# Kernel optimization log

Hardware: AMD Instinct MI355X
Metric: run time of the kernel (lower is better)

Reference implementation:

```python
import jax, jax.numpy as jnp
import numpy as np

B, C_ENC, H, W = 8, 512, 96, 96
N_SAMP = 64            # num_samples in forward
N_NODES = 2 * N_SAMP   # 64 pos + 64 neg per image
D = 256                # node feature dim after head_in_ln
N_HEADS = 8
DH = D // N_HEADS
SINKHORN_ITERS = 10


def _ln(x):
    # LayerNorm(elementwise_affine=False)
    m = x.mean(-1, keepdims=True)
    v = x.var(-1, keepdims=True)
    return (x - m) / jnp.sqrt(v + 1e-5)


def setup_inputs() -> dict:
    key = jax.random.key(0)
    ks = jax.random.split(key, 12)
    std = 0.01  # matches nn.init.normal_(std=0.01) in _init_weights
    inp = {
        "feat_s": jax.random.normal(ks[0], (B, C_ENC, H, W), jnp.float32),
        "score_s": jax.random.normal(ks[1], (B, 1, H, W), jnp.float32),
        "feat_t": jax.random.normal(ks[2], (B, C_ENC, H, W), jnp.float32),
        "score_t": jax.random.normal(ks[3], (B, 1, H, W), jnp.float32),
        "head_W1": std * jax.random.normal(ks[4], (C_ENC, D), jnp.float32),
        "head_b1": jnp.zeros((D,), jnp.float32),
        "head_W2": std * jax.random.normal(ks[5], (D, D), jnp.float32),
        "head_b2": jnp.zeros((D,), jnp.float32),
        "intra_W": jax.random.normal(ks[6], (4, D, D), jnp.float32) / jnp.sqrt(jnp.float32(D)),
        "intra_b": jnp.zeros((4, D), jnp.float32),
        "cross_W": jax.random.normal(ks[7], (4, D, D), jnp.float32) / jnp.sqrt(jnp.float32(D)),
        "cross_b": jnp.zeros((4, D), jnp.float32),
        "cls_W1": std * jax.random.normal(ks[8], (D, 128), jnp.float32),
        "cls_b1": jnp.zeros((128,), jnp.float32),
        "cls_W2": std * jax.random.normal(ks[9], (128, 1), jnp.float32),
        "cls_b2": jnp.zeros((1,), jnp.float32),
        "aff_A": jax.random.normal(ks[10], (D, D), jnp.float32) / jnp.sqrt(jnp.float32(D)),
    }
    return inp


def _sample_points(feat, score):
    # torch version: boolean-mask nonzero + random gather of 64 pos / 64 neg spatial
    # locations per image. JIT-friendly deterministic equivalent: top-64 highest
    # sigmoid scores = positives, top-64 lowest = negatives.
    s = jax.nn.sigmoid(score[:, 0].reshape(B, -1))            # [B, H*W]
    _, pos_idx = jax.lax.top_k(s, N_SAMP)
    _, neg_idx = jax.lax.top_k(-s, N_SAMP)
    idx = jnp.concatenate([pos_idx, neg_idx], axis=1)         # [B, 128]
    ff = feat.reshape(B, C_ENC, -1)                           # [B, 512, H*W]
    nodes = jnp.take_along_axis(ff, idx[:, None, :], axis=2)  # [B, 512, 128]
    nodes = nodes.transpose(0, 2, 1)                          # [B, 128, 512]
    labels = jnp.concatenate(
        [jnp.ones((B, N_SAMP, 1), feat.dtype), jnp.zeros((B, N_SAMP, 1), feat.dtype)], axis=1)
    return nodes, labels


def _mha(xq, xkv, Wp, bp):
    # standard multi-head attention (MultiHeadAttentionWrapper)
    q = xq @ Wp[0] + bp[0]
    k = xkv @ Wp[1] + bp[1]
    v = xkv @ Wp[2] + bp[2]
    sh = lambda t: t.reshape(t.shape[0], t.shape[1], N_HEADS, DH)
    att = jnp.einsum("bqhd,bkhd->bhqk", sh(q), sh(k)) / jnp.sqrt(jnp.float32(DH))
    att = jax.nn.softmax(att, axis=-1)
    o = jnp.einsum("bhqk,bkhd->bqhd", att, sh(v)).reshape(xq.shape[0], xq.shape[1], D)
    return o @ Wp[3] + bp[3], att.mean(1)


def _forward(feat_s, score_s, feat_t, score_t, head_W1, head_b1, head_W2, head_b2,
             intra_W, intra_b, cross_W, cross_b, cls_W1, cls_b1, cls_W2, cls_b2, aff_A):
    n1, l1 = _sample_points(feat_s, score_s)
    n2, l2 = _sample_points(feat_t, score_t)

    # head_in_ln: Linear -> LN -> ReLU -> Linear -> LN
    head = lambda x: _ln(jax.nn.relu(_ln(x @ head_W1 + head_b1)) @ head_W2 + head_b2)
    n1, n2 = head(n1), head(n2)

    # intra-domain graph (self-attention), shared weights for both domains
    n1, _ = _mha(n1, n1, intra_W, intra_b)
    n2, _ = _mha(n2, n2, intra_W, intra_b)

    # cross-domain graph (cross-attention both directions, shared weights)
    c1, _ = _mha(n1, n2, cross_W, cross_b)
    c2, _ = _mha(n2, n1, cross_W, cross_b)
    n1, n2 = c1, c2

    # node classification loss (BCEWithLogits, mean)
    cls = lambda x: jax.nn.relu(x @ cls_W1 + cls_b1) @ cls_W2 + cls_b2
    def bce_logits(logit, lab):
        return jnp.mean(jnp.maximum(logit, 0) - logit * lab + jnp.log1p(jnp.exp(-jnp.abs(logit))))
    node_loss = bce_logits(cls(n1), l1) + bce_logits(cls(n2), l2)

    # affinity + InstanceNorm2d(1) + sinkhorn refine
    Mmat = jnp.einsum("bnd,de,bme->bnm", n1, aff_A, n2)       # [B, 128, 128]
    mu = Mmat.mean((1, 2), keepdims=True)
    var = Mmat.var((1, 2), keepdims=True)
    K = (Mmat - mu) / jnp.sqrt(var + 1e-5)
    for _ in range(SINKHORN_ITERS):  # log-space row/col normalization
        K = K - jax.nn.logsumexp(K, axis=2, keepdims=True)
        K = K - jax.nn.logsumexp(K, axis=1, keepdims=True)
    P = jnp.exp(K)

    # matching loss = BCEFocalLoss(gamma=2, alpha=0.25) vs label-agreement matrix
    gt = (l1[:, :, 0][:, :, None] == l2[:, :, 0][:, None, :]).astype(P.dtype)
    pt = jnp.clip(P, 1e-6, 1.0 - 1e-6)
    mat_loss = jnp.mean(-0.25 * (1 - pt) ** 2 * gt * jnp.log(pt)
                        - 0.75 * pt ** 2 * (1 - gt) * jnp.log(1 - pt))

    total_loss = node_loss + 10.0 * mat_loss
    return n1, total_loss


def reference(feat_s, score_s, feat_t, score_t, head_W1, head_b1, head_W2, head_b2,
              intra_W, intra_b, cross_W, cross_b, cls_W1, cls_b1, cls_W2, cls_b2, aff_A):
    return _forward(feat_s, score_s, feat_t, score_t, head_W1, head_b1, head_W2, head_b2,
                    intra_W, intra_b, cross_W, cross_b, cls_W1, cls_b1, cls_W2, cls_b2, aff_A)
```

## Files before the change

kernel.cpp:

```cpp
#include <hip/hip_runtime.h>
#include <math.h>

#define BIMG 8
#define HW 9216
#define CENC 512
#define NN 128
#define DD 256
#define NHEAD 8
#define DH 32
#define ROWS1 1024
#define ROWS2 2048
#define TAILB 264

typedef unsigned long long ull;
typedef __attribute__((ext_vector_type(4))) float f32x4;
typedef __attribute__((ext_vector_type(4))) unsigned u32x4;
typedef __attribute__((ext_vector_type(2))) unsigned u32x2;

__device__ __forceinline__ unsigned short f2bf(float f) {
  unsigned u = __float_as_uint(f);
  u += 0x7fffu + ((u >> 16) & 1u);
  return (unsigned short)(u >> 16);
}
__device__ __forceinline__ float bf2f(unsigned h) { return __uint_as_float(h << 16); }
__device__ __forceinline__ unsigned pack2(float a, float b) {
  return (unsigned)f2bf(a) | ((unsigned)f2bf(b) << 16);
}

__device__ __forceinline__ ull cmpex_keep(ull k, ull o, bool keepMax) {
  return ((k > o) == keepMax) ? k : o;
}
__device__ __forceinline__ void bsort64(ull& k, int lane) {
#pragma unroll
  for (int size = 2; size <= 64; size <<= 1) {
#pragma unroll
    for (int stride = size >> 1; stride > 0; stride >>= 1) {
      ull o = __shfl_xor(k, stride);
      bool keepMax = (((lane & size) == 0) == ((lane & stride) == 0));
      k = cmpex_keep(k, o, keepMax);
    }
  }
}
__device__ __forceinline__ void bmerge64(ull& top, ull b, int lane) {
  ull rev = __shfl_xor(b, 63);
  ull m = top > rev ? top : rev;
#pragma unroll
  for (int stride = 32; stride > 0; stride >>= 1) {
    ull o = __shfl_xor(m, stride);
    m = cmpex_keep(m, o, (lane & stride) == 0);
  }
  top = m;
}

__global__ __launch_bounds__(256) void head_kernel(const float* __restrict__ score_s,
                                                   const float* __restrict__ score_t,
                                                   int* __restrict__ idx_out,
                                                   float* __restrict__ loss_acc,
                                                   const float* __restrict__ hw1,
                                                   const float* __restrict__ hw2,
                                                   const float* __restrict__ iw,
                                                   const float* __restrict__ cw,
                                                   const float* __restrict__ aw,
                                                   unsigned short* __restrict__ wt) {
  __shared__ ull sm[256];
  __shared__ float tile[32][33];
  int tid = threadIdx.x;
  if (blockIdx.x < 32) {
    int blk = blockIdx.x;
    int bi = blk >> 1, neg = blk & 1;
    int lane = tid & 63, w = tid >> 6;
    if (blk == 0 && tid < 4) loss_acc[tid] = 0.f;
    const float* sp = (bi < 8 ? score_s : score_t) + (size_t)(bi & 7) * HW;
    int q0 = w * 36;
    ull keys[36];
#pragma unroll
    for (int j = 0; j < 36; ++j) {
      float x = sp[(q0 + j) * 64 + lane];
      unsigned ub = __float_as_uint(x);
      unsigned u = (ub & 0x80000000u) ? ~ub : (ub | 0x80000000u);
      if (neg) u = ~u;
      int gi = (q0 + j) * 64 + lane;
      keys[j] = ((ull)u << 32) | (unsigned)(~gi);
    }
    ull top1 = keys[0];  bsort64(top1, lane);
    ull top2 = keys[18]; bsort64(top2, lane);
#pragma unroll
    for (int j = 1; j < 18; ++j) {
      ull k1 = keys[j], k2 = keys[18 + j];
      bsort64(k1, lane);
      bsort64(k2, lane);
      bmerge64(top1, k1, lane);
      bmerge64(top2, k2, lane);
    }
    bmerge64(top1, top2, lane);
    sm[w * 64 + lane] = top1;
    __syncthreads();
    if (w < 2) {
      ull a = sm[(2 * w) * 64 + lane];
      ull b = sm[(2 * w + 1) * 64 + (63 - lane)];
      ull m = a > b ? a : b;
#pragma unroll
      for (int stride = 32; stride > 0; stride >>= 1) {
        ull o = __shfl_xor(m, stride);
        m = cmpex_keep(m, o, (lane & stride) == 0);
      }
      sm[(2 * w) * 64 + lane] = m;
    }
    __syncthreads();
    if (w == 0) {
      ull a = sm[lane];
      ull b = sm[128 + (63 - lane)];
      ull m = a > b ? a : b;
#pragma unroll
      for (int stride = 32; stride > 0; stride >>= 1) {
        ull o = __shfl_xor(m, stride);
        m = cmpex_keep(m, o, (lane & stride) == 0);
      }
      idx_out[bi * NN + neg * 64 + lane] = (int)(~(unsigned)(m & 0xffffffffull));
    }
  } else {
    int bid = blockIdx.x - 32;
    const float* src; unsigned short* dst; int K, k0, n0;
    if (bid < 128) {
      src = hw1; dst = wt; K = 512;
      k0 = (bid >> 3) * 32; n0 = (bid & 7) * 32;
    } else {
      int id2 = bid - 128;
      int m = id2 >> 6, tt = id2 & 63;
      K = 256;
      k0 = (tt >> 3) * 32; n0 = (tt & 7) * 32;
      src = (m == 0) ? hw2 : (m < 5) ? iw + (size_t)(m - 1) * 65536
          : (m < 9) ? cw + (size_t)(m - 5) * 65536 : aw;
      dst = wt + 131072 + (size_t)m * 65536;
    }
    int r = tid >> 3, c = (tid & 7) * 4;
    float4 v = *(const float4*)&src[(size_t)(k0 + r) * 256 + n0 + c];
    tile[r][c] = v.x; tile[r][c + 1] = v.y; tile[r][c + 2] = v.z; tile[r][c + 3] = v.w;
    __syncthreads();
    u32x2 o;
    o[0] = pack2(tile[c][r], tile[c + 1][r]);
    o[1] = pack2(tile[c + 2][r], tile[c + 3][r]);
    *(u32x2*)&dst[(size_t)(n0 + r) * K + k0 + c] = o;
  }
}

__global__ __launch_bounds__(256) void gather_kernel(const float* __restrict__ feat_s,
                                                     const float* __restrict__ feat_t,
                                                     const int* __restrict__ idx,
                                                     unsigned short* __restrict__ nodes) {
  int blk = blockIdx.x;
  int bi = blk >> 7, n = blk & 127;
  int b = bi & 7;
  const float* fp = (bi < 8) ? feat_s : feat_t;
  int pos = idx[bi * NN + n];
  const float* src = fp + (size_t)b * CENC * HW + pos;
  unsigned* dst = (unsigned*)(nodes + (size_t)blk * CENC);
  int t = threadIdx.x;
  float f0 = src[(size_t)(2 * t) * HW];
  float f1 = src[(size_t)(2 * t + 1) * HW];
  dst[t] = pack2(f0, f1);
}

template<int K>
__global__ __launch_bounds__(256) void gemm_mf(const unsigned short* __restrict__ A,
                                               const unsigned short* __restrict__ Wt,
                                               const float* __restrict__ bias,
                                               unsigned short* __restrict__ Cb,
                                               float* __restrict__ Cf,
                                               int ldc, int f32rows,
                                               const float* __restrict__ in_stats, int in_relu,
                                               float* __restrict__ out_stats,
                                               int Az, int Wz, int Cbz, int Cfz, int bz) {
  constexpr int LDK = K + 8;
  constexpr int KC = K / 8;
  __shared__ unsigned short As[32][LDK];
  __shared__ unsigned short Bs[64][LDK];
  __shared__ float mS[32], rS[32];
  int z = blockIdx.z;
  A  += (size_t)z * Az;
  Wt += (size_t)z * Wz;
  if (Cb)   Cb += (size_t)z * Cbz;
  if (Cf)   Cf += (size_t)z * Cfz;
  if (bias) bias += (size_t)z * bz;
  int n0 = blockIdx.x * 64, m0 = blockIdx.y * 32;
  int t = threadIdx.x;
  if (in_stats) {
    if (t < 32) {
      const float* sp = in_stats + (size_t)(m0 + t) * 16;
      float s = 0.f, q = 0.f;
#pragma unroll
      for (int i = 0; i < 8; ++i) { s += sp[i]; q += sp[8 + i]; }
      float m = s * (1.0f / 256.f);
      float var = q * (1.0f / 256.f) - m * m;
      mS[t] = m;
      rS[t] = 1.0f / sqrtf(var + 1e-5f);
    }
    __syncthreads();
  }
  for (int i = t; i < 32 * KC; i += 256) {
    int row = i / KC, c8 = (i % KC) * 8;
    u32x4 av = *(const u32x4*)&A[(size_t)(m0 + row) * K + c8];
    if (in_stats) {
      float m = mS[row], r = rS[row];
#pragma unroll
      for (int j = 0; j < 4; ++j) {
        float f0 = (bf2f(av[j] & 0xffffu) - m) * r;
        float f1 = (bf2f(av[j] >> 16) - m) * r;
        if (in_relu) { f0 = fmaxf(f0, 0.f); f1 = fmaxf(f1, 0.f); }
        av[j] = pack2(f0, f1);
      }
    }
    *(u32x4*)&As[row][c8] = av;
  }
  for (int i = t; i < 64 * KC; i += 256) {
    int row = i / KC, c8 = (i % KC) * 8;
    *(u32x4*)&Bs[row][c8] = *(const u32x4*)&Wt[(size_t)(n0 + row) * K + c8];
  }
  __syncthreads();
  int l = t & 63, w = t >> 6;
  int wr = w >> 1, wc = w & 1;
  int fra = wr * 16 + (l & 15);
  int frk = (l >> 4) * 8;
  int fb0 = wc * 32 + (l & 15), fb1 = fb0 + 16;
  f32x4 acc0 = {0.f, 0.f, 0.f, 0.f};
  f32x4 acc1 = {0.f, 0.f, 0.f, 0.f};
#pragma unroll
  for (int ks = 0; ks < K / 32; ++ks) {
    u32x4 af = *(const u32x4*)&As[fra][ks * 32 + frk];
    u32x4 b0 = *(const u32x4*)&Bs[fb0][ks * 32 + frk];
    u32x4 b1 = *(const u32x4*)&Bs[fb1][ks * 32 + frk];
    asm volatile("v_mfma_f32_16x16x32_bf16 %0, %1, %2, %0" : "+v"(acc0) : "v"(af), "v"(b0));
    asm volatile("v_mfma_f32_16x16x32_bf16 %0, %1, %2, %0" : "+v"(acc1) : "v"(af), "v"(b1));
  }
  asm volatile("s_nop 7\n\ts_nop 7" ::);
  int col0 = n0 + wc * 32 + (l & 15);
  int rbase = m0 + wr * 16 + (l >> 4) * 4;
  float b0 = 0.f, b1 = 0.f;
  if (bias) { b0 = bias[col0]; b1 = bias[col0 + 16]; }
#pragma unroll
  for (int r = 0; r < 4; ++r) {
    int row = rbase + r;
    float o0 = acc0[r] + b0;
    float o1 = acc1[r] + b1;
    if (Cb) {
      Cb[(size_t)row * 256 + col0]      = f2bf(o0);
      Cb[(size_t)row * 256 + col0 + 16] = f2bf(o1);
    }
    if (Cf && row < f32rows) {
      Cf[(size_t)row * ldc + col0]      = o0;
      Cf[(size_t)row * ldc + col0 + 16] = o1;
    }
    if (out_stats) {
      float s = o0 + o1, q = o0 * o0 + o1 * o1;
#pragma unroll
      for (int m = 1; m < 16; m <<= 1) { s += __shfl_xor(s, m); q += __shfl_xor(q, m); }
      if ((l & 15) == 0) {
        out_stats[(size_t)row * 16 + blockIdx.x * 2 + wc]     = s;
        out_stats[(size_t)row * 16 + 8 + blockIdx.x * 2 + wc] = q;
      }
    }
  }
}

__global__ __launch_bounds__(256) void attn_kernel(const unsigned short* __restrict__ q,
                                                   const unsigned short* __restrict__ k,
                                                   const unsigned short* __restrict__ v,
                                                   unsigned short* __restrict__ o, int swap) {
  __shared__ __align__(16) float Ks[NN][DH];
  __shared__ __align__(16) float Vs[NN][DH];
  __shared__ __align__(16) float Ex[64][3][34];
  int blk = blockIdx.x;
  int bb = blk >> 4, h = (blk >> 1) & 7, qh = blk & 1;
  int kb = swap ? (bb ^ 8) : bb;
  int t = threadIdx.x;
  int rr = t & 63, part = t >> 6;
  for (int e = t; e < 1024; e += 256) {
    int which = e >> 9;
    int idx2 = e & 511;
    int r = idx2 >> 2, c8 = (idx2 & 3) * 8;
    u32x4 val = *(const u32x4*)&(which ? v : k)[(size_t)(kb * NN + r) * DD + h * DH + c8];
    float* dst = which ? &Vs[r][c8] : &Ks[r][c8];
#pragma unroll
    for (int i = 0; i < 4; ++i) {
      dst[2 * i]     = bf2f(val[i] & 0xffffu);
      dst[2 * i + 1] = bf2f(val[i] >> 16);
    }
  }
  __syncthreads();
  int qrow = bb * NN + qh * 64 + rr;
  float4 q4[8];
  {
    const unsigned short* qp = q + (size_t)qrow * DD + h * DH;
#pragma unroll
    for (int c4 = 0; c4 < 4; ++c4) {
      u32x4 u = *(const u32x4*)&qp[c4 * 8];
      q4[c4 * 2].x = bf2f(u[0] & 0xffffu); q4[c4 * 2].y = bf2f(u[0] >> 16);
      q4[c4 * 2].z = bf2f(u[1] & 0xffffu); q4[c4 * 2].w = bf2f(u[1] >> 16);
      q4[c4 * 2 + 1].x = bf2f(u[2] & 0xffffu); q4[c4 * 2 + 1].y = bf2f(u[2] >> 16);
      q4[c4 * 2 + 1].z = bf2f(u[3] & 0xffffu); q4[c4 * 2 + 1].w = bf2f(u[3] >> 16);
    }
  }
  const float scale = 0.17677669529663687f;
  int j0 = part * 32;
  float mx = -1e30f;
  for (int j = j0; j < j0 + 32; ++j) {
    const float4* kp = (const float4*)Ks[j];
    float s = 0.f;
#pragma unroll
    for (int c4 = 0; c4 < 8; ++c4) {
      float4 kv = kp[c4];
      s += q4[c4].x * kv.x + q4[c4].y * kv.y + q4[c4].z * kv.z + q4[c4].w * kv.w;
    }
    mx = fmaxf(mx, s * scale);
  }
  float acc[DH];
#pragma unroll
  for (int c = 0; c < DH; ++c) acc[c] = 0.f;
  float den = 0.f;
  for (int j = j0; j < j0 + 32; ++j) {
    const float4* kp = (const float4*)Ks[j];
    float s = 0.f;
#pragma unroll
    for (int c4 = 0; c4 < 8; ++c4) {
      float4 kv = kp[c4];
      s += q4[c4].x * kv.x + q4[c4].y * kv.y + q4[c4].z * kv.z + q4[c4].w * kv.w;
    }
    float e = expf(s * scale - mx);
    den += e;
    const float4* vp = (const float4*)Vs[j];
#pragma unroll
    for (int c4 = 0; c4 < 8; ++c4) {
      float4 vv = vp[c4];
      acc[c4 * 4 + 0] += e * vv.x; acc[c4 * 4 + 1] += e * vv.y;
      acc[c4 * 4 + 2] += e * vv.z; acc[c4 * 4 + 3] += e * vv.w;
    }
  }
  if (part) {
#pragma unroll
    for (int c = 0; c < DH; ++c) Ex[rr][part - 1][c] = acc[c];
    Ex[rr][part - 1][32] = mx;
    Ex[rr][part - 1][33] = den;
  }
  __syncthreads();
  if (part == 0) {
    float M = mx;
#pragma unroll
    for (int p = 0; p < 3; ++p) M = fmaxf(M, Ex[rr][p][32]);
    float f0 = expf(mx - M);
    float fp[3];
    float dt = den * f0;
#pragma unroll
    for (int p = 0; p < 3; ++p) { fp[p] = expf(Ex[rr][p][32] - M); dt += Ex[rr][p][33] * fp[p]; }
    float inv = 1.0f / dt;
    unsigned ovu[16];
#pragma unroll
    for (int c = 0; c < 16; ++c) {
      float x0 = acc[2 * c] * f0, x1 = acc[2 * c + 1] * f0;
#pragma unroll
      for (int p = 0; p < 3; ++p) { x0 += Ex[rr][p][2 * c] * fp[p]; x1 += Ex[rr][p][2 * c + 1] * fp[p]; }
      ovu[c] = pack2(x0 * inv, x1 * inv);
    }
    unsigned* op = (unsigned*)(o + (size_t)qrow * DD + h * DH);
#pragma unroll
    for (int i = 0; i < 4; ++i) {
      u32x4 w4;
      w4[0] = ovu[4 * i]; w4[1] = ovu[4 * i + 1]; w4[2] = ovu[4 * i + 2]; w4[3] = ovu[4 * i + 3];
      *(u32x4*)&op[4 * i] = w4;
    }
  }
}

struct SkSmem {
  unsigned short tmpL[128][264];
  float Km[128][132];
  float u_[NN];
  float v_[NN];
  float red[20];
};
struct ClsSmem {
  float xs[8][256];
  float red[16];
};
union TailSmem { SkSmem sk; ClsSmem cls; };

__device__ __forceinline__ void ticket_finalize(float* acc, float* out) {
  __threadfence();
  int tk = atomicAdd((int*)acc + 3, 1);
  if (tk == TAILB - 1) {
    float a0 = atomicAdd(acc + 0, 0.0f);
    float a1 = atomicAdd(acc + 1, 0.0f);
    out[ROWS1 * DD] = a0 + 10.0f * a1;
  }
}

__global__ __launch_bounds__(1024) void tail_kernel(const unsigned short* __restrict__ bufH,
                                                    const unsigned short* __restrict__ wt_af,
                                                    const float* __restrict__ W1,
                                                    const float* __restrict__ b1,
                                                    const float* __restrict__ W2,
                                                    const float* __restrict__ b2,
                                                    float* __restrict__ acc,
                                                    float* __restrict__ out) {
  __shared__ TailSmem sm;
  int t = threadIdx.x;
  int bid = blockIdx.x;
  if (bid < 8) {
    int b = bid;
    int l = t & 63, w = t >> 6;
    int tr = w >> 1;
    const unsigned short* c1 = bufH + (size_t)(b * 128) * 256;
    const unsigned short* c2 = bufH + (size_t)(1024 + b * 128) * 256;
    {
      int tcB = (w & 1) * 8;
      f32x4 accA[8];
#pragma unroll
      for (int i = 0; i < 8; ++i) accA[i] = (f32x4){0.f, 0.f, 0.f, 0.f};
      for (int ks = 0; ks < 8; ++ks) {
        int kk = ks * 32 + (l >> 4) * 8;
        u32x4 af = *(const u32x4*)&c1[(size_t)(tr * 16 + (l & 15)) * 256 + kk];
#pragma unroll
        for (int i = 0; i < 8; ++i) {
          u32x4 bf = *(const u32x4*)&wt_af[(size_t)((tcB + i) * 16 + (l & 15)) * 256 + kk];
          asm volatile("v_mfma_f32_16x16x32_bf16 %0, %1, %2, %0" : "+v"(accA[i]) : "v"(af), "v"(bf));
        }
      }
      asm volatile("s_nop 7\n\ts_nop 7" ::);
      int rb = tr * 16 + (l >> 4) * 4;
#pragma unroll
      for (int i = 0; i < 8; ++i) {
        int col = (tcB + i) * 16 + (l & 15);
#pragma unroll
        for (int r = 0; r < 4; ++r)
          sm.sk.tmpL[rb + r][col] = f2bf(accA[i][r]);
      }
    }
    __syncthreads();
    {
      int tcB = (w & 1) * 4;
      f32x4 accB[4];
#pragma unroll
      for (int i = 0; i < 4; ++i) accB[i] = (f32x4){0.f, 0.f, 0.f, 0.f};
      for (int ks = 0; ks < 8; ++ks) {
        int kk = ks * 32 + (l >> 4) * 8;
        u32x4 af = *(const u32x4*)&sm.sk.tmpL[tr * 16 + (l & 15)][kk];
#pragma unroll
        for (int i = 0; i < 4; ++i) {
          u32x4 bf = *(const u32x4*)&c2[(size_t)((tcB + i) * 16 + (l & 15)) * 256 + kk];
          asm volatile("v_mfma_f32_16x16x32_bf16 %0, %1, %2, %0" : "+v"(accB[i]) : "v"(af), "v"(bf));
        }
      }
      asm volatile("s_nop 7\n\ts_nop 7" ::);
      int rb = tr * 16 + (l >> 4) * 4;
#pragma unroll
      for (int i = 0; i < 4; ++i) {
        int col = (tcB + i) * 16 + (l & 15);
#pragma unroll
        for (int r = 0; r < 4; ++r)
          sm.sk.Km[rb + r][col] = accB[i][r];
      }
    }
    __syncthreads();
    int r = t >> 3, cg = t & 7;
    int c = t >> 3, rg = t & 7;
    float kr[16], kc[16];
    {
#pragma unroll
      for (int q4 = 0; q4 < 4; ++q4) {
        float4 f = *(const float4*)&sm.sk.Km[r][cg * 16 + q4 * 4];
        kr[q4 * 4 + 0] = f.x; kr[q4 * 4 + 1] = f.y; kr[q4 * 4 + 2] = f.z; kr[q4 * 4 + 3] = f.w;
      }
#pragma unroll
      for (int q = 0; q < 16; ++q)
        kc[q] = sm.sk.Km[rg * 16 + q][c];
    }
    float s = 0.f;
#pragma unroll
    for (int q = 0; q < 16; ++q) s += kr[q];
    for (int m = 1; m < 64; m <<= 1) s += __shfl_xor(s, m);
    if ((t & 63) == 0) sm.sk.red[t >> 6] = s;
    __syncthreads();
    if (t == 0) { float tt = 0.f; for (int i = 0; i < 16; ++i) tt += sm.sk.red[i]; sm.sk.red[16] = tt; }
    __syncthreads();
    float mu = sm.sk.red[16] * (1.0f / 16384.f);
    __syncthreads();
    float sq = 0.f;
#pragma unroll
    for (int q = 0; q < 16; ++q) { float d = kr[q] - mu; sq += d * d; }
    for (int m = 1; m < 64; m <<= 1) sq += __shfl_xor(sq, m);
    if ((t & 63) == 0) sm.sk.red[t >> 6] = sq;
    __syncthreads();
    if (t == 0) { float tt = 0.f; for (int i = 0; i < 16; ++i) tt += sm.sk.red[i]; sm.sk.red[17] = tt; }
    __syncthreads();
    float inv = 1.0f / sqrtf(sm.sk.red[17] * (1.0f / 16384.f) + 1e-5f);
#pragma unroll
    for (int q = 0; q < 16; ++q) { kr[q] = (kr[q] - mu) * inv; kc[q] = (kc[q] - mu) * inv; }
    if (t < NN) { sm.sk.u_[t] = 0.f; sm.sk.v_[t] = 0.f; }
    __syncthreads();
    for (int iter = 0; iter < 10; ++iter) {
      float tmp[16];
      {
        const float4* vp = (const float4*)(sm.sk.v_ + cg * 16);
#pragma unroll
        for (int q4 = 0; q4 < 4; ++q4) {
          float4 f = vp[q4];
          tmp[q4 * 4 + 0] = kr[q4 * 4 + 0] - f.x; tmp[q4 * 4 + 1] = kr[q4 * 4 + 1] - f.y;
          tmp[q4 * 4 + 2] = kr[q4 * 4 + 2] - f.z; tmp[q4 * 4 + 3] = kr[q4 * 4 + 3] - f.w;
        }
        float mx = tmp[0];
#pragma unroll
        for (int q = 1; q < 16; ++q) mx = fmaxf(mx, tmp[q]);
        for (int m = 1; m < 8; m <<= 1) mx = fmaxf(mx, __shfl_xor(mx, m));
        float smv = 0.f;
#pragma unroll
        for (int q = 0; q < 16; ++q) smv += expf(tmp[q] - mx);
        for (int m = 1; m < 8; m <<= 1) smv += __shfl_xor(smv, m);
        if (cg == 0) sm.sk.u_[r] = mx + logf(smv);
      }
      __syncthreads();
      {
        const float4* up = (const float4*)(sm.sk.u_ + rg * 16);
#pragma unroll
        for (int q4 = 0; q4 < 4; ++q4) {
          float4 f = up[q4];
          tmp[q4 * 4 + 0] = kc[q4 * 4 + 0] - f.x; tmp[q4 * 4 + 1] = kc[q4 * 4 + 1] - f.y;
          tmp[q4 * 4 + 2] = kc[q4 * 4 + 2] - f.z; tmp[q4 * 4 + 3] = kc[q4 * 4 + 3] - f.w;
        }
        float mx = tmp[0];
#pragma unroll
        for (int q = 1; q < 16; ++q) mx = fmaxf(mx, tmp[q]);
        for (int m = 1; m < 8; m <<= 1) mx = fmaxf(mx, __shfl_xor(mx, m));
        float smv = 0.f;
#pragma unroll
        for (int q = 0; q < 16; ++q) smv += expf(tmp[q] - mx);
        for (int m = 1; m < 8; m <<= 1) smv += __shfl_xor(smv, m);
        if (rg == 0) sm.sk.v_[c] = mx + logf(smv);
      }
      __syncthreads();
    }
    float ur = sm.sk.u_[r];
    float fsum = 0.f;
    {
      const float4* vp = (const float4*)(sm.sk.v_ + cg * 16);
#pragma unroll
      for (int q4 = 0; q4 < 4; ++q4) {
        float4 f = vp[q4];
        float vv[4] = {f.x, f.y, f.z, f.w};
#pragma unroll
        for (int j = 0; j < 4; ++j) {
          float P = expf(kr[q4 * 4 + j] - ur - vv[j]);
          float pt = fminf(fmaxf(P, 1e-6f), 1.0f - 1e-6f);
          int col = cg * 16 + q4 * 4 + j;
          bool gt = (r < 64) == (col < 64);
          float wgt = gt ? (-0.25f * (1.f - pt) * (1.f - pt)) : (-0.75f * pt * pt);
          float lg = gt ? logf(pt) : logf(1.f - pt);
          fsum += wgt * lg;
        }
      }
    }
    for (int m = 1; m < 64; m <<= 1) fsum += __shfl_xor(fsum, m);
    if ((t & 63) == 0) sm.sk.red[t >> 6] = fsum;
    __syncthreads();
    if (t == 0) {
      float tt = 0.f; for (int i = 0; i < 16; ++i) tt += sm.sk.red[i];
      atomicAdd(acc + 1, tt * (1.0f / 131072.f));
      ticket_finalize(acc, out);
    }
  } else {
    int row0 = (bid - 8) * 8;
    int col = t & 127, grp = t >> 7;
    if (t < 256) {
      int rr = t >> 5, c8 = (t & 31) * 8;
      u32x4 u = *(const u32x4*)&bufH[(size_t)(row0 + rr) * 256 + c8];
#pragma unroll
      for (int i = 0; i < 4; ++i) {
        sm.cls.xs[rr][c8 + 2 * i]     = bf2f(u[i] & 0xffffu);
        sm.cls.xs[rr][c8 + 2 * i + 1] = bf2f(u[i] >> 16);
      }
    }
    __syncthreads();
    float h = b1[col];
    for (int kk = 0; kk < 256; ++kk)
      h += sm.cls.xs[grp][kk] * W1[kk * 128 + col];
    float p = fmaxf(h, 0.f) * W2[col];
#pragma unroll
    for (int m = 1; m < 64; m <<= 1) p += __shfl_xor(p, m);
    if ((t & 63) == 0) sm.cls.red[t >> 6] = p;
    __syncthreads();
    if (t == 0) {
      float total = 0.f;
      float bb2 = b2[0];
#pragma unroll
      for (int g = 0; g < 8; ++g) {
        float z = sm.cls.red[2 * g] + sm.cls.red[2 * g + 1] + bb2;
        float lab = (((row0 + g) & 127) < 64) ? 1.f : 0.f;
        total += fmaxf(z, 0.f) - z * lab + log1pf(expf(-fabsf(z)));
      }
      atomicAdd(acc, total * (1.0f / 1024.0f));
      ticket_finalize(acc, out);
    }
  }
}

extern "C" void kernel_launch(void* const* d_in, const int* in_sizes, int n_in,
                              void* d_out, int out_size, void* d_ws, size_t ws_size,
                              hipStream_t stream) {
  const float* feat_s  = (const float*)d_in[0];
  const float* score_s = (const float*)d_in[1];
  const float* feat_t  = (const float*)d_in[2];
  const float* score_t = (const float*)d_in[3];
  const float* head_W1 = (const float*)d_in[4];
  const float* head_b1 = (const float*)d_in[5];
  const float* head_W2 = (const float*)d_in[6];
  const float* head_b2 = (const float*)d_in[7];
  const float* intra_W = (const float*)d_in[8];
  const float* intra_b = (const float*)d_in[9];
  const float* cross_W = (const float*)d_in[10];
  const float* cross_b = (const float*)d_in[11];
  const float* cls_W1  = (const float*)d_in[12];
  const float* cls_b1  = (const float*)d_in[13];
  const float* cls_W2  = (const float*)d_in[14];
  const float* cls_b2  = (const float*)d_in[15];
  const float* aff_A   = (const float*)d_in[16];

  unsigned short* nodes_bf = (unsigned short*)d_ws;
  unsigned short* bufA_bf  = nodes_bf + 2048 * 512;
  unsigned short* bufB_bf  = bufA_bf + ROWS2 * DD;
  unsigned short* bufH_bf  = bufB_bf + ROWS2 * DD;
  unsigned short* qkv_bf   = bufH_bf + ROWS2 * DD;
  unsigned short* attn_bf  = qkv_bf + 3 * ROWS2 * DD;
  unsigned short* wt       = attn_bf + ROWS2 * DD;
  float* st1  = (float*)(wt + 786432);
  float* st2  = st1 + ROWS2 * 16;
  float* acc  = st2 + ROWS2 * 16;
  int*   idxb = (int*)(acc + 8);
  float* out_f = (float*)d_out;

  unsigned short* wt_h1 = wt;
  unsigned short* wt_h2 = wt + 131072;
  unsigned short* wt_in = wt_h2 + 65536;
  unsigned short* wt_cr = wt_in + 4 * 65536;
  unsigned short* wt_af = wt_cr + 4 * 65536;

  head_kernel<<<800, 256, 0, stream>>>(score_s, score_t, idxb, acc,
                                       head_W1, head_W2, intra_W, cross_W, aff_A, wt);
  gather_kernel<<<2048, 256, 0, stream>>>(feat_s, feat_t, idxb, nodes_bf);

  dim3 g1(4, 64, 1);
  dim3 gq(4, 64, 3);
  const float* nulf = nullptr;
  float* nulw = nullptr;

  gemm_mf<512><<<g1, 256, 0, stream>>>(nodes_bf, wt_h1, head_b1, bufA_bf, nulw,
                                       0, 0, nulf, 0, st1, 0, 0, 0, 0, 0);
  gemm_mf<256><<<g1, 256, 0, stream>>>(bufA_bf, wt_h2, head_b2, bufB_bf, nulw,
                                       0, 0, st1, 1, st2, 0, 0, 0, 0, 0);
  gemm_mf<256><<<gq, 256, 0, stream>>>(bufB_bf, wt_in, intra_b, qkv_bf, nulw,
                                       0, 0, st2, 0, nulw, 0, 65536, ROWS2 * DD, 0, 256);
  attn_kernel<<<256, 256, 0, stream>>>(qkv_bf, qkv_bf + ROWS2 * DD, qkv_bf + 2 * ROWS2 * DD,
                                       attn_bf, 0);
  gemm_mf<256><<<g1, 256, 0, stream>>>(attn_bf, wt_in + 3 * 65536, intra_b + 768, bufH_bf, nulw,
                                       0, 0, nulf, 0, nulw, 0, 0, 0, 0, 0);
  gemm_mf<256><<<gq, 256, 0, stream>>>(bufH_bf, wt_cr, cross_b, qkv_bf, nulw,
                                       0, 0, nulf, 0, nulw, 0, 65536, ROWS2 * DD, 0, 256);
  attn_kernel<<<256, 256, 0, stream>>>(qkv_bf, qkv_bf + ROWS2 * DD, qkv_bf + 2 * ROWS2 * DD,
                                       attn_bf, 1);
  gemm_mf<256><<<g1, 256, 0, stream>>>(attn_bf, wt_cr + 3 * 65536, cross_b + 768, bufH_bf, out_f,
                                       256, ROWS1, nulf, 0, nulw, 0, 0, 0, 0, 0);
  tail_kernel<<<TAILB, 1024, 0, stream>>>(bufH_bf, wt_af, cls_W1, cls_b1, cls_W2, cls_b2,
                                          acc, out_f);
}
```

Before: 235.6 us.

## Pre-transpose classifier weights to bf16, split tail cls blocks finer, use fast exp/log

The head kernel now gets extra blocks that transpose cls_W1 into a bf16 column-major buffer. The tail classifier reads that buffer with vectorized 16-byte loads, handles 4 rows per block instead of 8, and splits K into two halves across threads, so it launches twice as many blocks. The Sinkhorn shared-memory arrays tmpL and Km are put in a union, which needs an extra barrier, and expf/logf become __expf/__logf in attention and the tail. In exchange it adds bf16 rounding of cls_W1 and lower-accuracy intrinsics.

```diff
diff --git a/kernel.cpp b/kernel.cpp
--- a/kernel.cpp
+++ b/kernel.cpp
@@ -10,7 +10,7 @@
 #define DH 32
 #define ROWS1 1024
 #define ROWS2 2048
-#define TAILB 264
+#define TAILB 520
 
 typedef unsigned long long ull;
 typedef __attribute__((ext_vector_type(4))) float f32x4;
@@ -61,7 +61,9 @@
                                                    const float* __restrict__ iw,
                                                    const float* __restrict__ cw,
                                                    const float* __restrict__ aw,
-                                                   unsigned short* __restrict__ wt) {
+                                                   const float* __restrict__ clsW1,
+                                                   unsigned short* __restrict__ wt,
+                                                   unsigned short* __restrict__ w1t) {
   __shared__ ull sm[256];
   __shared__ float tile[32][33];
   int tid = threadIdx.x;
@@ -118,7 +120,7 @@
       }
       idx_out[bi * NN + neg * 64 + lane] = (int)(~(unsigned)(m & 0xffffffffull));
     }
-  } else {
+  } else if (blockIdx.x < 800) {
     int bid = blockIdx.x - 32;
     const float* src; unsigned short* dst; int K, k0, n0;
     if (bid < 128) {
@@ -141,6 +143,17 @@
     o[0] = pack2(tile[c][r], tile[c + 1][r]);
     o[1] = pack2(tile[c + 2][r], tile[c + 3][r]);
     *(u32x2*)&dst[(size_t)(n0 + r) * K + k0 + c] = o;
+  } else {
+    int bid3 = blockIdx.x - 800;
+    int k0 = (bid3 >> 2) * 32, n0 = (bid3 & 3) * 32;
+    int r = tid >> 3, c = (tid & 7) * 4;
+    float4 v = *(const float4*)&clsW1[(size_t)(k0 + r) * 128 + n0 + c];
+    tile[r][c] = v.x; tile[r][c + 1] = v.y; tile[r][c + 2] = v.z; tile[r][c + 3] = v.w;
+    __syncthreads();
+    u32x2 o;
+    o[0] = pack2(tile[c][r], tile[c + 1][r]);
+    o[1] = pack2(tile[c + 2][r], tile[c + 3][r]);
+    *(u32x2*)&w1t[(size_t)(n0 + r) * 256 + k0 + c] = o;
   }
 }
 
@@ -325,7 +338,7 @@
       float4 kv = kp[c4];
       s += q4[c4].x * kv.x + q4[c4].y * kv.y + q4[c4].z * kv.z + q4[c4].w * kv.w;
     }
-    float e = expf(s * scale - mx);
+    float e = __expf(s * scale - mx);
     den += e;
     const float4* vp = (const float4*)Vs[j];
 #pragma unroll
@@ -346,11 +359,11 @@
     float M = mx;
 #pragma unroll
     for (int p = 0; p < 3; ++p) M = fmaxf(M, Ex[rr][p][32]);
-    float f0 = expf(mx - M);
+    float f0 = __expf(mx - M);
     float fp[3];
     float dt = den * f0;
 #pragma unroll
-    for (int p = 0; p < 3; ++p) { fp[p] = expf(Ex[rr][p][32] - M); dt += Ex[rr][p][33] * fp[p]; }
+    for (int p = 0; p < 3; ++p) { fp[p] = __expf(Ex[rr][p][32] - M); dt += Ex[rr][p][33] * fp[p]; }
     float inv = 1.0f / dt;
     unsigned ovu[16];
 #pragma unroll
@@ -371,15 +384,15 @@
 }
 
 struct SkSmem {
-  unsigned short tmpL[128][264];
-  float Km[128][132];
+  union { unsigned short tmpL[128][264]; float Km[128][132]; } u;
   float u_[NN];
   float v_[NN];
   float red[20];
 };
 struct ClsSmem {
-  float xs[8][256];
-  float red[16];
+  float xs[4][256];
+  float part[4][128];
+  float red[8];
 };
 union TailSmem { SkSmem sk; ClsSmem cls; };
 
@@ -395,7 +408,7 @@
 
 __global__ __launch_bounds__(1024) void tail_kernel(const unsigned short* __restrict__ bufH,
                                                     const unsigned short* __restrict__ wt_af,
-                                                    const float* __restrict__ W1,
+                                                    const unsigned short* __restrict__ w1t,
                                                     const float* __restrict__ b1,
                                                     const float* __restrict__ W2,
                                                     const float* __restrict__ b2,
@@ -431,18 +444,18 @@
         int col = (tcB + i) * 16 + (l & 15);
 #pragma unroll
         for (int r = 0; r < 4; ++r)
-          sm.sk.tmpL[rb + r][col] = f2bf(accA[i][r]);
-      }
-    }
-    __syncthreads();
+          sm.sk.u.tmpL[rb + r][col] = f2bf(accA[i][r]);
+      }
+    }
+    __syncthreads();
+    f32x4 accB[4];
     {
       int tcB = (w & 1) * 4;
-      f32x4 accB[4];
 #pragma unroll
       for (int i = 0; i < 4; ++i) accB[i] = (f32x4){0.f, 0.f, 0.f, 0.f};
       for (int ks = 0; ks < 8; ++ks) {
         int kk = ks * 32 + (l >> 4) * 8;
-        u32x4 af = *(const u32x4*)&sm.sk.tmpL[tr * 16 + (l & 15)][kk];
+        u32x4 af = *(const u32x4*)&sm.sk.u.tmpL[tr * 16 + (l & 15)][kk];
 #pragma unroll
         for (int i = 0; i < 4; ++i) {
           u32x4 bf = *(const u32x4*)&c2[(size_t)((tcB + i) * 16 + (l & 15)) * 256 + kk];
@@ -450,13 +463,17 @@
         }
       }
       asm volatile("s_nop 7\n\ts_nop 7" ::);
+    }
+    __syncthreads();
+    {
+      int tcB = (w & 1) * 4;
       int rb = tr * 16 + (l >> 4) * 4;
 #pragma unroll
       for (int i = 0; i < 4; ++i) {
         int col = (tcB + i) * 16 + (l & 15);
 #pragma unroll
         for (int r = 0; r < 4; ++r)
-          sm.sk.Km[rb + r][col] = accB[i][r];
+          sm.sk.u.Km[rb + r][col] = accB[i][r];
       }
     }
     __syncthreads();
@@ -466,12 +483,12 @@
     {
 #pragma unroll
       for (int q4 = 0; q4 < 4; ++q4) {
-        float4 f = *(const float4*)&sm.sk.Km[r][cg * 16 + q4 * 4];
+        float4 f = *(const float4*)&sm.sk.u.Km[r][cg * 16 + q4 * 4];
         kr[q4 * 4 + 0] = f.x; kr[q4 * 4 + 1] = f.y; kr[q4 * 4 + 2] = f.z; kr[q4 * 4 + 3] = f.w;
       }
 #pragma unroll
       for (int q = 0; q < 16; ++q)
-        kc[q] = sm.sk.Km[rg * 16 + q][c];
+        kc[q] = sm.sk.u.Km[rg * 16 + q][c];
     }
     float s = 0.f;
 #pragma unroll
@@ -512,9 +529,9 @@
         for (int m = 1; m < 8; m <<= 1) mx = fmaxf(mx, __shfl_xor(mx, m));
         float smv = 0.f;
 #pragma unroll
-        for (int q = 0; q < 16; ++q) smv += expf(tmp[q] - mx);
+        for (int q = 0; q < 16; ++q) smv += __expf(tmp[q] - mx);
         for (int m = 1; m < 8; m <<= 1) smv += __shfl_xor(smv, m);
-        if (cg == 0) sm.sk.u_[r] = mx + logf(smv);
+        if (cg == 0) sm.sk.u_[r] = mx + __logf(smv);
       }
       __syncthreads();
       {
@@ -531,9 +548,9 @@
         for (int m = 1; m < 8; m <<= 1) mx = fmaxf(mx, __shfl_xor(mx, m));
         float smv = 0.f;
 #pragma unroll
-        for (int q = 0; q < 16; ++q) smv += expf(tmp[q] - mx);
+        for (int q = 0; q < 16; ++q) smv += __expf(tmp[q] - mx);
         for (int m = 1; m < 8; m <<= 1) smv += __shfl_xor(smv, m);
-        if (rg == 0) sm.sk.v_[c] = mx + logf(smv);
+        if (rg == 0) sm.sk.v_[c] = mx + __logf(smv);
       }
       __syncthreads();
     }
@@ -547,12 +564,12 @@
         float vv[4] = {f.x, f.y, f.z, f.w};
 #pragma unroll
         for (int j = 0; j < 4; ++j) {
-          float P = expf(kr[q4 * 4 + j] - ur - vv[j]);
+          float P = __expf(kr[q4 * 4 + j] - ur - vv[j]);
           float pt = fminf(fmaxf(P, 1e-6f), 1.0f - 1e-6f);
           int col = cg * 16 + q4 * 4 + j;
           bool gt = (r < 64) == (col < 64);
           float wgt = gt ? (-0.25f * (1.f - pt) * (1.f - pt)) : (-0.75f * pt * pt);
-          float lg = gt ? logf(pt) : logf(1.f - pt);
+          float lg = gt ? __logf(pt) : __logf(1.f - pt);
           fsum += wgt * lg;
         }
       }
@@ -566,34 +583,43 @@
       ticket_finalize(acc, out);
     }
   } else {
-    int row0 = (bid - 8) * 8;
-    int col = t & 127, grp = t >> 7;
-    if (t < 256) {
-      int rr = t >> 5, c8 = (t & 31) * 8;
-      u32x4 u = *(const u32x4*)&bufH[(size_t)(row0 + rr) * 256 + c8];
-#pragma unroll
-      for (int i = 0; i < 4; ++i) {
-        sm.cls.xs[rr][c8 + 2 * i]     = bf2f(u[i] & 0xffffu);
-        sm.cls.xs[rr][c8 + 2 * i + 1] = bf2f(u[i] >> 16);
-      }
-    }
-    __syncthreads();
-    float h = b1[col];
-    for (int kk = 0; kk < 256; ++kk)
-      h += sm.cls.xs[grp][kk] * W1[kk * 128 + col];
-    float p = fmaxf(h, 0.f) * W2[col];
-#pragma unroll
-    for (int m = 1; m < 64; m <<= 1) p += __shfl_xor(p, m);
-    if ((t & 63) == 0) sm.cls.red[t >> 6] = p;
+    int row0 = (bid - 8) * 4;
+    {
+      int rr = t >> 8, cc = t & 255;
+      sm.cls.xs[rr][cc] = bf2f(bufH[(size_t)(row0 + rr) * 256 + cc]);
+    }
+    __syncthreads();
+    int grp = t >> 8, col = t & 127, kh = (t >> 7) & 1;
+    const unsigned short* wp = w1t + (size_t)col * 256 + kh * 128;
+    const float* xp = &sm.cls.xs[grp][kh * 128];
+    float h = 0.f;
+#pragma unroll
+    for (int i = 0; i < 16; ++i) {
+      u32x4 wv = *(const u32x4*)&wp[i * 8];
+      const float* x8 = xp + i * 8;
+      h += x8[0] * bf2f(wv[0] & 0xffffu) + x8[1] * bf2f(wv[0] >> 16)
+         + x8[2] * bf2f(wv[1] & 0xffffu) + x8[3] * bf2f(wv[1] >> 16)
+         + x8[4] * bf2f(wv[2] & 0xffffu) + x8[5] * bf2f(wv[2] >> 16)
+         + x8[6] * bf2f(wv[3] & 0xffffu) + x8[7] * bf2f(wv[3] >> 16);
+    }
+    if (kh == 1) sm.cls.part[grp][col] = h;
+    __syncthreads();
+    if (kh == 0) {
+      float z = h + sm.cls.part[grp][col] + b1[col];
+      float p = fmaxf(z, 0.f) * W2[col];
+#pragma unroll
+      for (int m = 1; m < 64; m <<= 1) p += __shfl_xor(p, m);
+      if ((t & 63) == 0) sm.cls.red[grp * 2 + ((t >> 6) & 1)] = p;
+    }
     __syncthreads();
     if (t == 0) {
       float total = 0.f;
       float bb2 = b2[0];
 #pragma unroll
-      for (int g = 0; g < 8; ++g) {
+      for (int g = 0; g < 4; ++g) {
         float z = sm.cls.red[2 * g] + sm.cls.red[2 * g + 1] + bb2;
         float lab = (((row0 + g) & 127) < 64) ? 1.f : 0.f;
-        total += fmaxf(z, 0.f) - z * lab + log1pf(expf(-fabsf(z)));
+        total += fmaxf(z, 0.f) - z * lab + log1pf(__expf(-fabsf(z)));
       }
       atomicAdd(acc, total * (1.0f / 1024.0f));
       ticket_finalize(acc, out);
@@ -629,7 +655,8 @@
   unsigned short* qkv_bf   = bufH_bf + ROWS2 * DD;
   unsigned short* attn_bf  = qkv_bf + 3 * ROWS2 * DD;
   unsigned short* wt       = attn_bf + ROWS2 * DD;
-  float* st1  = (float*)(wt + 786432);
+  unsigned short* w1t      = wt + 786432;
+  float* st1  = (float*)(w1t + 32768);
   float* st2  = st1 + ROWS2 * 16;
   float* acc  = st2 + ROWS2 * 16;
   int*   idxb = (int*)(acc + 8);
@@ -641,8 +668,9 @@
   unsigned short* wt_cr = wt_in + 4 * 65536;
   unsigned short* wt_af = wt_cr + 4 * 65536;
 
-  head_kernel<<<800, 256, 0, stream>>>(score_s, score_t, idxb, acc,
-                                       head_W1, head_W2, intra_W, cross_W, aff_A, wt);
+  head_kernel<<<832, 256, 0, stream>>>(score_s, score_t, idxb, acc,
+                                       head_W1, head_W2, intra_W, cross_W, aff_A, cls_W1,
+                                       wt, w1t);
   gather_kernel<<<2048, 256, 0, stream>>>(feat_s, feat_t, idxb, nodes_bf);
 
   dim3 g1(4, 64, 1);
@@ -666,6 +694,6 @@
                                        attn_bf, 1);
   gemm_mf<256><<<g1, 256, 0, stream>>>(attn_bf, wt_cr + 3 * 65536, cross_b + 768, bufH_bf, out_f,
                                        256, ROWS1, nulf, 0, nulw, 0, 0, 0, 0, 0);
-  tail_kernel<<<TAILB, 1024, 0, stream>>>(bufH_bf, wt_af, cls_W1, cls_b1, cls_W2, cls_b2,
+  tail_kernel<<<TAILB, 1024, 0, stream>>>(bufH_bf, wt_af, w1t, cls_b1, cls_W2, cls_b2,
                                           acc, out_f);
 }
```

Result: faster. 217.7 us (-7.6%).
